# Kernel tuning notes

Measured on AMD Instinct MI355X. Metric: run time of the kernel, lower is better.

Reference implementation:

```python
import jax, jax.numpy as jnp
import numpy as np

B, T, EMB, HEAD = 8, 4096, 1024, 64  # batch, seq (=block_sz), emb_dim, head_sz


def setup_inputs() -> dict:
    key = jax.random.key(0)
    kx, kw = jax.random.split(key)
    x = jax.random.normal(kx, (B, T, EMB), dtype=jnp.float32)
    W = jax.random.normal(kw, (EMB, 3 * HEAD), dtype=jnp.float32) * 0.02
    return {"x": x, "W": W}


def reference(x, W):
    # fused QKV projection: [B,T,EMB] @ [EMB,3*HEAD] -> [B,T,3*HEAD]
    kqv = x @ W
    k, q, v = jnp.split(kqv, 3, axis=-1)  # source order: k, q, v
    head_sz = q.shape[-1]
    # causal attention scores: [B,T,T]
    scores = jnp.einsum('btd,bsd->bts', q, k) / jnp.sqrt(jnp.float32(head_sz))
    causal_mask = jnp.triu(jnp.full((scores.shape[1], scores.shape[2]), -jnp.inf, dtype=scores.dtype), 1)
    w = jax.nn.softmax(scores + causal_mask, axis=-1)
    # dropout p=0.0 -> identity
    out = jnp.einsum('bts,bsd->btd', w, v)  # [B,T,HEAD]
    return out
```

## Files before the change

### kernel.cpp

```cpp
#include <hip/hip_runtime.h>
#include <hip/hip_bf16.h>

#define BATCH 8
#define SEQ 4096
#define EMB 1024
#define HEAD 64
#define N3 192

#define BM 64
#define BK 64
#define NT (EMB / BK)
#define LSTR 72

typedef __attribute__((ext_vector_type(4))) float f32x4;
typedef __attribute__((ext_vector_type(8))) short bf16x8;
typedef __attribute__((ext_vector_type(4))) short short4v;
typedef __attribute__((ext_vector_type(4))) float float4v;
typedef __attribute__((ext_vector_type(2))) unsigned int u32x2;

#define LOG2E 1.4426950408889634f
#define QSCALE (0.125f * LOG2E)


static __device__ __forceinline__ unsigned short f2bf(float f) {
  unsigned int x = __builtin_bit_cast(unsigned int, f);
  x += 0x7fffu + ((x >> 16) & 1u);
  return (unsigned short)(x >> 16);
}

__global__ __launch_bounds__(256) void wt_kernel(const float* __restrict__ W,
                                                 unsigned short* __restrict__ Wt) {
  int idx = blockIdx.x * 256 + threadIdx.x;
  int k = idx / N3, c = idx % N3;
  Wt[(size_t)c * EMB + k] = f2bf(W[idx]);
}

__global__ __launch_bounds__(256, 2) void qkv_kernel(const float* __restrict__ x,
                                                     const unsigned short* __restrict__ Wt,
                                                     unsigned short* __restrict__ PK,
                                                     unsigned short* __restrict__ PQ,
                                                     unsigned short* __restrict__ PV) {
  __shared__ unsigned short Asm[2][BM][LSTR];
  __shared__ unsigned short Bsm[2][N3][LSTR];

  const int tid = threadIdx.x;
  const int wid = tid >> 6;
  const int lane = tid & 63;
  const int l16 = lane & 15;
  const int lg = lane >> 4;
  const int m0 = blockIdx.x * BM;

  const int ar0 = tid >> 4;
  const int ac4 = tid & 15;
  const int br0 = tid >> 3;
  const int bc = tid & 7;

  const float* xa = x + (size_t)(m0 + ar0) * EMB + ac4 * 4;
  const unsigned short* wb = Wt + (size_t)br0 * EMB + bc * 8;

  f32x4 acc[4][3];
#pragma unroll
  for (int mi = 0; mi < 4; ++mi)
#pragma unroll
    for (int ni = 0; ni < 3; ++ni) acc[mi][ni] = (f32x4)0.0f;

  float4v av[4];
  bf16x8 bv[6];

#define ISSUE_LOADS(K0)                                                        \
  {                                                                            \
    _Pragma("unroll") for (int i = 0; i < 4; ++i)                              \
        av[i] = *(const float4v*)(xa + (size_t)(16 * i) * EMB + (K0));         \
    _Pragma("unroll") for (int i = 0; i < 6; ++i)                              \
        bv[i] = *(const bf16x8*)(wb + (size_t)(32 * i) * EMB + (K0));          \
  }

#define WRITE_LDS(BUF)                                                         \
  {                                                                            \
    _Pragma("unroll") for (int i = 0; i < 4; ++i) {                            \
      short4v p;                                                               \
      _Pragma("unroll") for (int j = 0; j < 4; ++j)                            \
          p[j] = (short)f2bf(av[i][j]);                                        \
      *(short4v*)&Asm[BUF][ar0 + 16 * i][ac4 * 4] = p;                         \
    }                                                                          \
    _Pragma("unroll") for (int i = 0; i < 6; ++i)                              \
        *(bf16x8*)&Bsm[BUF][br0 + 32 * i][bc * 8] = bv[i];                     \
  }

#define COMPUTE(BUF)                                                           \
  {                                                                            \
    _Pragma("unroll") for (int kh = 0; kh < 2; ++kh) {                         \
      bf16x8 af[4], bfr[3];                                                    \
      _Pragma("unroll") for (int mi = 0; mi < 4; ++mi)                         \
          af[mi] = *(const bf16x8*)&Asm[BUF][mi * 16 + l16][kh * 32 + lg * 8]; \
      _Pragma("unroll") for (int ni = 0; ni < 3; ++ni)                         \
          bfr[ni] = *(const bf16x8*)&Bsm[BUF][wid * 48 + ni * 16 + l16][kh * 32 + lg * 8]; \
      _Pragma("unroll") for (int mi = 0; mi < 4; ++mi)                         \
        _Pragma("unroll") for (int ni = 0; ni < 3; ++ni)                       \
            acc[mi][ni] = __builtin_amdgcn_mfma_f32_16x16x32_bf16(             \
                af[mi], bfr[ni], acc[mi][ni], 0, 0, 0);                        \
    }                                                                          \
  }

  ISSUE_LOADS(0)
  WRITE_LDS(0)
  __syncthreads();

  int cur = 0;
  for (int t = 0; t < NT; ++t) {
    if (t < NT - 1) ISSUE_LOADS((t + 1) * BK)
    COMPUTE(cur)
    if (t < NT - 1) {
      WRITE_LDS(cur ^ 1)
    }
    __syncthreads();
    cur ^= 1;
  }
#undef ISSUE_LOADS
#undef WRITE_LDS
#undef COMPUTE

#pragma unroll
  for (int mi = 0; mi < 4; ++mi) {
#pragma unroll
    for (int ni = 0; ni < 3; ++ni) {
      const int n = wid * 48 + ni * 16 + l16;
#pragma unroll
      for (int r = 0; r < 4; ++r) {
        const int row = m0 + mi * 16 + lg * 4 + r;
        const int bb = row >> 12;
        const int ss = row & (SEQ - 1);
        const float v = acc[mi][ni][r];
        if (n < 64) {
          PK[(((size_t)bb * 256 + (ss >> 4)) * 2 + (n >> 5)) * 512 +
             (ss & 15) * 32 + (n & 31)] = f2bf(v);
        } else if (n < 128) {
          const int d = n - 64;
          PQ[(((size_t)bb * 256 + (ss >> 4)) * 2 + (d >> 5)) * 512 +
             (ss & 15) * 32 + (d & 31)] = f2bf(v * QSCALE);
        } else {
          const int d = n - 128;
          PV[(((size_t)bb * 64 + (ss >> 6)) * 8 + (d >> 4) * 2 + ((ss >> 5) & 1)) * 512 +
             (d & 15) * 32 + (ss & 31)] = f2bf(v);
        }
      }
    }
  }
}

__global__ __launch_bounds__(256, 2) void attn_kernel(const unsigned short* __restrict__ PK,
                                                      const unsigned short* __restrict__ PQ,
                                                      const unsigned short* __restrict__ PV,
                                                      float* __restrict__ out) {
  __shared__ float Msm[4][16];
  __shared__ float Lsm[4][16];
  __shared__ float Osm[4][4][16][17];
  __shared__ unsigned short Pl[4][2][16][LSTR];

  const int tid = threadIdx.x;
  const int wid = tid >> 6;
  const int lane = tid & 63;
  const int l16 = lane & 15;
  const int lg = lane >> 4;
  const int lam = (l16 * 4 + lg) * 8;

  const int Bid = blockIdx.x;
  const int b = Bid & 7;
  const int idx = Bid >> 3;
  const int i_ = idx & 31;
  const int u = (idx >> 5) ? (63 - i_) : i_;
  const int q0 = u * 64;
  const int T_total = u + 1;
  const int t0 = (wid * T_total) >> 2;
  const int t1 = ((wid + 1) * T_total) >> 2;

  const unsigned short* pqb = PQ + (size_t)b * 256 * 1024;

  bf16x8 qf[4][2];
#pragma unroll
  for (int c = 0; c < 4; ++c) {
    qf[c][0] = *(const bf16x8*)(pqb + ((size_t)(4 * u + c) * 2 + 0) * 512 + lam);
    qf[c][1] = *(const bf16x8*)(pqb + ((size_t)(4 * u + c) * 2 + 1) * 512 + lam);
  }

  f32x4 oC[4][4];
  float m_[4], l_[4];
#pragma unroll
  for (int c = 0; c < 4; ++c) {
    m_[c] = -3.0e38f; l_[c] = 0.0f;
#pragma unroll
    for (int dd = 0; dd < 4; ++dd) oC[c][dd] = (f32x4)0.0f;
  }

  const unsigned short* kp = PK + (size_t)b * 256 * 1024 + (size_t)t0 * 4096 + lam;
  const unsigned short* vp = PV + (size_t)b * 64 * 8 * 512 + (size_t)t0 * 4096 + lam;

  for (int it = t0; it < t1; ++it) {
    const int kv0 = it << 6;

    bf16x8 kf[8], vf[8];
#pragma unroll
    for (int t = 0; t < 4; ++t) {
      kf[2 * t] = *(const bf16x8*)(kp + t * 1024);
      kf[2 * t + 1] = *(const bf16x8*)(kp + t * 1024 + 512);
    }
#pragma unroll
    for (int dd = 0; dd < 4; ++dd) {
      vf[2 * dd] = *(const bf16x8*)(vp + dd * 1024);
      vf[2 * dd + 1] = *(const bf16x8*)(vp + dd * 1024 + 512);
    }

#pragma unroll
    for (int c = 0; c < 4; ++c) {
      const int q0c = q0 + 16 * c;

      f32x4 s[4];
      __builtin_amdgcn_s_setprio(1);
#pragma unroll
      for (int t = 0; t < 4; ++t) {
        f32x4 z = (f32x4)0.0f;
        z = __builtin_amdgcn_mfma_f32_16x16x32_bf16(kf[2 * t], qf[c][0], z, 0, 0, 0);
        s[t] = __builtin_amdgcn_mfma_f32_16x16x32_bf16(kf[2 * t + 1], qf[c][1], z, 0, 0, 0);
      }
      __builtin_amdgcn_s_setprio(0);

      if (kv0 + 64 > q0c) {
        const int base = kv0 + lg * 4 - q0c - l16;
#pragma unroll
        for (int t = 0; t < 4; ++t)
#pragma unroll
          for (int r = 0; r < 4; ++r)
            if (base + 16 * t + r > 0) s[t][r] = -3.0e38f;
      }

      {
        float mx = s[0][0];
#pragma unroll
        for (int t = 0; t < 4; ++t)
#pragma unroll
          for (int r = 0; r < 4; ++r) mx = fmaxf(mx, s[t][r]);
        mx = fmaxf(mx, __shfl_xor(mx, 16));
        mx = fmaxf(mx, __shfl_xor(mx, 32));
        if (!__all(mx <= m_[c])) {
          float mn = fmaxf(m_[c], mx);
          float al = exp2f(m_[c] - mn);
          m_[c] = mn; l_[c] *= al;
#pragma unroll
          for (int dd = 0; dd < 4; ++dd) oC[c][dd] *= al;
        }
        float ps = 0.0f;
#pragma unroll
        for (int t = 0; t < 4; ++t) {
          float p0 = exp2f(s[t][0] - m_[c]);
          float p1 = exp2f(s[t][1] - m_[c]);
          float p2 = exp2f(s[t][2] - m_[c]);
          float p3 = exp2f(s[t][3] - m_[c]);
          ps += (p0 + p1) + (p2 + p3);
          u32x2 w;
          w[0] = (__builtin_bit_cast(unsigned int, p1) & 0xFFFF0000u) |
                 (__builtin_bit_cast(unsigned int, p0) >> 16);
          w[1] = (__builtin_bit_cast(unsigned int, p3) & 0xFFFF0000u) |
                 (__builtin_bit_cast(unsigned int, p2) >> 16);
          *(u32x2*)&Pl[wid][c & 1][l16][16 * t + lg * 4] = w;
        }
        ps += __shfl_xor(ps, 16);
        ps += __shfl_xor(ps, 32);
        l_[c] += ps;
      }

      {
        bf16x8 pf0 = *(const bf16x8*)&Pl[wid][c & 1][l16][lg * 8];
        bf16x8 pf1 = *(const bf16x8*)&Pl[wid][c & 1][l16][32 + lg * 8];
        __builtin_amdgcn_s_setprio(1);
#pragma unroll
        for (int dd = 0; dd < 4; ++dd) {
          oC[c][dd] = __builtin_amdgcn_mfma_f32_16x16x32_bf16(vf[2 * dd], pf0, oC[c][dd], 0, 0, 0);
          oC[c][dd] = __builtin_amdgcn_mfma_f32_16x16x32_bf16(vf[2 * dd + 1], pf1, oC[c][dd], 0, 0, 0);
        }
        __builtin_amdgcn_s_setprio(0);
      }
    }

    kp += 4096;
    vp += 4096;
  }

#pragma unroll
  for (int c = 0; c < 4; ++c) {
    if (lg == 0) { Msm[wid][l16] = m_[c]; Lsm[wid][l16] = l_[c]; }
#pragma unroll
    for (int dd = 0; dd < 4; ++dd)
#pragma unroll
      for (int r = 0; r < 4; ++r)
        Osm[wid][dd][lg * 4 + r][l16] = oC[c][dd][r];
    __syncthreads();
    if (wid == 0) {
      float M = Msm[0][l16];
#pragma unroll
      for (int w = 1; w < 4; ++w) M = fmaxf(M, Msm[w][l16]);
      float L = 0.0f;
      f32x4 oc[4];
#pragma unroll
      for (int dd = 0; dd < 4; ++dd) oc[dd] = (f32x4)0.0f;
#pragma unroll
      for (int w = 0; w < 4; ++w) {
        float sc = exp2f(Msm[w][l16] - M);
        L += Lsm[w][l16] * sc;
#pragma unroll
        for (int dd = 0; dd < 4; ++dd)
#pragma unroll
          for (int r = 0; r < 4; ++r)
            oc[dd][r] += Osm[w][dd][lg * 4 + r][l16] * sc;
      }
      const float inv = 1.0f / L;
      float* op = out + ((size_t)b * SEQ + q0 + 16 * c + l16) * HEAD;
#pragma unroll
      for (int dd = 0; dd < 4; ++dd)
#pragma unroll
        for (int r = 0; r < 4; ++r)
          op[16 * dd + lg * 4 + r] = oc[dd][r] * inv;
    }
    __syncthreads();
  }
}

extern "C" void kernel_launch(void* const* d_in, const int* in_sizes, int n_in,
                              void* d_out, int out_size, void* d_ws, size_t ws_size,
                              hipStream_t stream) {
  (void)in_sizes; (void)n_in; (void)out_size; (void)ws_size;
  const float* x = (const float*)d_in[0];
  const float* W = (const float*)d_in[1];
  float* out = (float*)d_out;

  const size_t MB4 = (size_t)4 * 1024 * 1024;
  unsigned short* Wt = (unsigned short*)d_ws;
  unsigned short* PK = (unsigned short*)((char*)d_ws + 512 * 1024);
  unsigned short* PQ = (unsigned short*)((char*)d_ws + 512 * 1024 + MB4);
  unsigned short* PV = (unsigned short*)((char*)d_ws + 512 * 1024 + 2 * MB4);

  hipLaunchKernelGGL(wt_kernel, dim3((EMB * N3) / 256), dim3(256), 0, stream, W, Wt);
  hipLaunchKernelGGL(qkv_kernel, dim3((BATCH * SEQ) / BM), dim3(256), 0, stream, x, Wt, PK, PQ, PV);
  hipLaunchKernelGGL(attn_kernel, dim3(BATCH * 64), dim3(256), 0, stream, PK, PQ, PV, out);
}
```

Measured before the change: 91.78 us.

## Restructure attention: per-wave query chunks with shared LDS-staged K/V double buffer

The attention kernel no longer splits the KV range across waves with a final cross-wave merge. Each wave now owns one 16-row query chunk and walks the full causal KV range. K/V tiles are staged cooperatively into a double-buffered LDS tile using global_load_lds, so all four waves share them. Further changes: native exp2, perm-based bf16 packing, vectorized output stores, and launch bounds raised to 4 blocks per CU. This removes the merge, its LDS traffic and the syncs. In exchange it adds a per-iteration block barrier, and waves with fewer causal tiles idle at the barrier less efficiently.

Measured after the change: 116.6 us. 1.27x slower.

```diff
diff --git a/kernel.cpp b/kernel.cpp
--- a/kernel.cpp
+++ b/kernel.cpp
@@ -21,6 +21,9 @@
 #define LOG2E 1.4426950408889634f
 #define QSCALE (0.125f * LOG2E)
 
+#define FEXP2(x) __builtin_amdgcn_exp2f(x)
+#define BFPACK(a, b) __builtin_amdgcn_perm(__builtin_bit_cast(unsigned int, (b)), \
+                                           __builtin_bit_cast(unsigned int, (a)), 0x07060302u)
 
 static __device__ __forceinline__ unsigned short f2bf(float f) {
   unsigned int x = __builtin_bit_cast(unsigned int, f);
@@ -148,14 +151,13 @@
   }
 }
 
-__global__ __launch_bounds__(256, 2) void attn_kernel(const unsigned short* __restrict__ PK,
+__global__ __launch_bounds__(256, 4) void attn_kernel(const unsigned short* __restrict__ PK,
                                                       const unsigned short* __restrict__ PQ,
                                                       const unsigned short* __restrict__ PV,
                                                       float* __restrict__ out) {
-  __shared__ float Msm[4][16];
-  __shared__ float Lsm[4][16];
-  __shared__ float Osm[4][4][16][17];
-  __shared__ unsigned short Pl[4][2][16][LSTR];
+  __shared__ unsigned short Ksm[2][4096];
+  __shared__ unsigned short Vsm[2][4096];
+  __shared__ unsigned short Pl[4][16][LSTR];
 
   const int tid = threadIdx.x;
   const int wid = tid >> 6;
@@ -163,164 +165,136 @@
   const int l16 = lane & 15;
   const int lg = lane >> 4;
   const int lam = (l16 * 4 + lg) * 8;
+  const int wq = wid * 1024;
 
   const int Bid = blockIdx.x;
   const int b = Bid & 7;
   const int idx = Bid >> 3;
   const int i_ = idx & 31;
   const int u = (idx >> 5) ? (63 - i_) : i_;
-  const int q0 = u * 64;
-  const int T_total = u + 1;
-  const int t0 = (wid * T_total) >> 2;
-  const int t1 = ((wid + 1) * T_total) >> 2;
-
+  const int T = u + 1;
+  const int qc = 4 * u + wid;
+  const int q0c = qc * 16;
+
+  const unsigned short* pkb = PK + (size_t)b * 256 * 1024;
+  const unsigned short* pvb = PV + (size_t)b * 64 * 8 * 512;
   const unsigned short* pqb = PQ + (size_t)b * 256 * 1024;
 
-  bf16x8 qf[4][2];
-#pragma unroll
-  for (int c = 0; c < 4; ++c) {
-    qf[c][0] = *(const bf16x8*)(pqb + ((size_t)(4 * u + c) * 2 + 0) * 512 + lam);
-    qf[c][1] = *(const bf16x8*)(pqb + ((size_t)(4 * u + c) * 2 + 1) * 512 + lam);
-  }
-
-  f32x4 oC[4][4];
-  float m_[4], l_[4];
-#pragma unroll
-  for (int c = 0; c < 4; ++c) {
-    m_[c] = -3.0e38f; l_[c] = 0.0f;
-#pragma unroll
-    for (int dd = 0; dd < 4; ++dd) oC[c][dd] = (f32x4)0.0f;
-  }
-
-  const unsigned short* kp = PK + (size_t)b * 256 * 1024 + (size_t)t0 * 4096 + lam;
-  const unsigned short* vp = PV + (size_t)b * 64 * 8 * 512 + (size_t)t0 * 4096 + lam;
-
-  for (int it = t0; it < t1; ++it) {
+  bf16x8 qf0 = *(const bf16x8*)(pqb + ((size_t)qc * 2 + 0) * 512 + lam);
+  bf16x8 qf1 = *(const bf16x8*)(pqb + ((size_t)qc * 2 + 1) * 512 + lam);
+
+  f32x4 o[4];
+#pragma unroll
+  for (int dd = 0; dd < 4; ++dd) o[dd] = (f32x4)0.0f;
+  float m_ = -3.0e38f, lsum = 0.0f;
+
+#define STAGE(T_, BUF)                                                         \
+  {                                                                            \
+    const unsigned short* gk = pkb + (size_t)(T_) * 4096 + wq + lane * 8;      \
+    const unsigned short* gv = pvb + (size_t)(T_) * 4096 + wq + lane * 8;      \
+    __builtin_amdgcn_global_load_lds(                                          \
+        (const __attribute__((address_space(1))) void*)gk,                     \
+        (__attribute__((address_space(3))) void*)&Ksm[BUF][wq], 16, 0, 0);     \
+    __builtin_amdgcn_global_load_lds(                                          \
+        (const __attribute__((address_space(1))) void*)(gk + 512),             \
+        (__attribute__((address_space(3))) void*)&Ksm[BUF][wq + 512], 16, 0, 0); \
+    __builtin_amdgcn_global_load_lds(                                          \
+        (const __attribute__((address_space(1))) void*)gv,                     \
+        (__attribute__((address_space(3))) void*)&Vsm[BUF][wq], 16, 0, 0);     \
+    __builtin_amdgcn_global_load_lds(                                          \
+        (const __attribute__((address_space(1))) void*)(gv + 512),             \
+        (__attribute__((address_space(3))) void*)&Vsm[BUF][wq + 512], 16, 0, 0); \
+  }
+
+  STAGE(0, 0)
+  __syncthreads();
+
+  for (int it = 0; it < T; ++it) {
+    const int buf = it & 1;
     const int kv0 = it << 6;
 
-    bf16x8 kf[8], vf[8];
+    if (it + 1 < T) STAGE(it + 1, buf ^ 1)
+
+    f32x4 s[4];
+    __builtin_amdgcn_s_setprio(1);
 #pragma unroll
     for (int t = 0; t < 4; ++t) {
-      kf[2 * t] = *(const bf16x8*)(kp + t * 1024);
-      kf[2 * t + 1] = *(const bf16x8*)(kp + t * 1024 + 512);
-    }
-#pragma unroll
-    for (int dd = 0; dd < 4; ++dd) {
-      vf[2 * dd] = *(const bf16x8*)(vp + dd * 1024);
-      vf[2 * dd + 1] = *(const bf16x8*)(vp + dd * 1024 + 512);
-    }
-
-#pragma unroll
-    for (int c = 0; c < 4; ++c) {
-      const int q0c = q0 + 16 * c;
-
-      f32x4 s[4];
+      bf16x8 kfa = *(const bf16x8*)&Ksm[buf][(2 * t) * 512 + lam];
+      bf16x8 kfb = *(const bf16x8*)&Ksm[buf][(2 * t + 1) * 512 + lam];
+      f32x4 z = (f32x4)0.0f;
+      z = __builtin_amdgcn_mfma_f32_16x16x32_bf16(kfa, qf0, z, 0, 0, 0);
+      s[t] = __builtin_amdgcn_mfma_f32_16x16x32_bf16(kfb, qf1, z, 0, 0, 0);
+    }
+    __builtin_amdgcn_s_setprio(0);
+
+    if (kv0 + 64 > q0c) {
+      const int base = kv0 + lg * 4 - q0c - l16;
+#pragma unroll
+      for (int t = 0; t < 4; ++t)
+#pragma unroll
+        for (int r = 0; r < 4; ++r)
+          if (base + 16 * t + r > 0) s[t][r] = -3.0e38f;
+    }
+
+    {
+      float mx = s[0][0];
+#pragma unroll
+      for (int t = 0; t < 4; ++t)
+#pragma unroll
+        for (int r = 0; r < 4; ++r) mx = fmaxf(mx, s[t][r]);
+      mx = fmaxf(mx, __shfl_xor(mx, 16));
+      mx = fmaxf(mx, __shfl_xor(mx, 32));
+      if (!__all(mx <= m_)) {
+        float mn = fmaxf(m_, mx);
+        float al = FEXP2(m_ - mn);
+        m_ = mn; lsum *= al;
+#pragma unroll
+        for (int dd = 0; dd < 4; ++dd) o[dd] *= al;
+      }
+      float ps = 0.0f;
+#pragma unroll
+      for (int t = 0; t < 4; ++t) {
+        float p0 = FEXP2(s[t][0] - m_);
+        float p1 = FEXP2(s[t][1] - m_);
+        float p2 = FEXP2(s[t][2] - m_);
+        float p3 = FEXP2(s[t][3] - m_);
+        ps += (p0 + p1) + (p2 + p3);
+        u32x2 w;
+        w[0] = BFPACK(p0, p1);
+        w[1] = BFPACK(p2, p3);
+        *(u32x2*)&Pl[wid][l16][16 * t + lg * 4] = w;
+      }
+      ps += __shfl_xor(ps, 16);
+      ps += __shfl_xor(ps, 32);
+      lsum += ps;
+    }
+
+    {
+      bf16x8 pf0 = *(const bf16x8*)&Pl[wid][l16][lg * 8];
+      bf16x8 pf1 = *(const bf16x8*)&Pl[wid][l16][32 + lg * 8];
       __builtin_amdgcn_s_setprio(1);
 #pragma unroll
-      for (int t = 0; t < 4; ++t) {
-        f32x4 z = (f32x4)0.0f;
-        z = __builtin_amdgcn_mfma_f32_16x16x32_bf16(kf[2 * t], qf[c][0], z, 0, 0, 0);
-        s[t] = __builtin_amdgcn_mfma_f32_16x16x32_bf16(kf[2 * t + 1], qf[c][1], z, 0, 0, 0);
+      for (int dd = 0; dd < 4; ++dd) {
+        bf16x8 vfa = *(const bf16x8*)&Vsm[buf][(2 * dd) * 512 + lam];
+        bf16x8 vfb = *(const bf16x8*)&Vsm[buf][(2 * dd + 1) * 512 + lam];
+        o[dd] = __builtin_amdgcn_mfma_f32_16x16x32_bf16(vfa, pf0, o[dd], 0, 0, 0);
+        o[dd] = __builtin_amdgcn_mfma_f32_16x16x32_bf16(vfb, pf1, o[dd], 0, 0, 0);
       }
       __builtin_amdgcn_s_setprio(0);
-
-      if (kv0 + 64 > q0c) {
-        const int base = kv0 + lg * 4 - q0c - l16;
-#pragma unroll
-        for (int t = 0; t < 4; ++t)
-#pragma unroll
-          for (int r = 0; r < 4; ++r)
-            if (base + 16 * t + r > 0) s[t][r] = -3.0e38f;
-      }
-
-      {
-        float mx = s[0][0];
-#pragma unroll
-        for (int t = 0; t < 4; ++t)
-#pragma unroll
-          for (int r = 0; r < 4; ++r) mx = fmaxf(mx, s[t][r]);
-        mx = fmaxf(mx, __shfl_xor(mx, 16));
-        mx = fmaxf(mx, __shfl_xor(mx, 32));
-        if (!__all(mx <= m_[c])) {
-          float mn = fmaxf(m_[c], mx);
-          float al = exp2f(m_[c] - mn);
-          m_[c] = mn; l_[c] *= al;
-#pragma unroll
-          for (int dd = 0; dd < 4; ++dd) oC[c][dd] *= al;
-        }
-        float ps = 0.0f;
-#pragma unroll
-        for (int t = 0; t < 4; ++t) {
-          float p0 = exp2f(s[t][0] - m_[c]);
-          float p1 = exp2f(s[t][1] - m_[c]);
-          float p2 = exp2f(s[t][2] - m_[c]);
-          float p3 = exp2f(s[t][3] - m_[c]);
-          ps += (p0 + p1) + (p2 + p3);
-          u32x2 w;
-          w[0] = (__builtin_bit_cast(unsigned int, p1) & 0xFFFF0000u) |
-                 (__builtin_bit_cast(unsigned int, p0) >> 16);
-          w[1] = (__builtin_bit_cast(unsigned int, p3) & 0xFFFF0000u) |
-                 (__builtin_bit_cast(unsigned int, p2) >> 16);
-          *(u32x2*)&Pl[wid][c & 1][l16][16 * t + lg * 4] = w;
-        }
-        ps += __shfl_xor(ps, 16);
-        ps += __shfl_xor(ps, 32);
-        l_[c] += ps;
-      }
-
-      {
-        bf16x8 pf0 = *(const bf16x8*)&Pl[wid][c & 1][l16][lg * 8];
-        bf16x8 pf1 = *(const bf16x8*)&Pl[wid][c & 1][l16][32 + lg * 8];
-        __builtin_amdgcn_s_setprio(1);
-#pragma unroll
-        for (int dd = 0; dd < 4; ++dd) {
-          oC[c][dd] = __builtin_amdgcn_mfma_f32_16x16x32_bf16(vf[2 * dd], pf0, oC[c][dd], 0, 0, 0);
-          oC[c][dd] = __builtin_amdgcn_mfma_f32_16x16x32_bf16(vf[2 * dd + 1], pf1, oC[c][dd], 0, 0, 0);
-        }
-        __builtin_amdgcn_s_setprio(0);
-      }
-    }
-
-    kp += 4096;
-    vp += 4096;
-  }
-
-#pragma unroll
-  for (int c = 0; c < 4; ++c) {
-    if (lg == 0) { Msm[wid][l16] = m_[c]; Lsm[wid][l16] = l_[c]; }
-#pragma unroll
-    for (int dd = 0; dd < 4; ++dd)
-#pragma unroll
-      for (int r = 0; r < 4; ++r)
-        Osm[wid][dd][lg * 4 + r][l16] = oC[c][dd][r];
+    }
+
     __syncthreads();
-    if (wid == 0) {
-      float M = Msm[0][l16];
-#pragma unroll
-      for (int w = 1; w < 4; ++w) M = fmaxf(M, Msm[w][l16]);
-      float L = 0.0f;
-      f32x4 oc[4];
-#pragma unroll
-      for (int dd = 0; dd < 4; ++dd) oc[dd] = (f32x4)0.0f;
-#pragma unroll
-      for (int w = 0; w < 4; ++w) {
-        float sc = exp2f(Msm[w][l16] - M);
-        L += Lsm[w][l16] * sc;
-#pragma unroll
-        for (int dd = 0; dd < 4; ++dd)
-#pragma unroll
-          for (int r = 0; r < 4; ++r)
-            oc[dd][r] += Osm[w][dd][lg * 4 + r][l16] * sc;
-      }
-      const float inv = 1.0f / L;
-      float* op = out + ((size_t)b * SEQ + q0 + 16 * c + l16) * HEAD;
-#pragma unroll
-      for (int dd = 0; dd < 4; ++dd)
-#pragma unroll
-        for (int r = 0; r < 4; ++r)
-          op[16 * dd + lg * 4 + r] = oc[dd][r] * inv;
-    }
-    __syncthreads();
+  }
+#undef STAGE
+
+  const float inv = 1.0f / lsum;
+  float* op = out + ((size_t)b * SEQ + q0c + l16) * HEAD;
+#pragma unroll
+  for (int dd = 0; dd < 4; ++dd) {
+    float4v v;
+#pragma unroll
+    for (int r = 0; r < 4; ++r) v[r] = o[dd][r] * inv;
+    *(float4v*)&op[16 * dd + lg * 4] = v;
   }
 }
 
```
